# Performance work log

Hardware: AMD Instinct MI355X
Metric: run time of the kernel (lower is better)

Reference implementation:

```python
import jax, jax.numpy as jnp
import numpy as np

B, N, D = 2, 1024, 1024
H, DH = 16, 64          # nhead, head_dim (D = H*DH)
FF = 4096               # dim_feedforward = 4*D
E = 8                   # num experts
EPS = 1e-5


def layer_norm(x, s, b):
    m = jnp.mean(x, -1, keepdims=True)
    v = jnp.mean((x - m) ** 2, -1, keepdims=True)
    return (x - m) * jax.lax.rsqrt(v + EPS) * s + b


def moe_gate(x, Wg):
    # top-1 gating: expert index + gate probability per token
    probs = jax.nn.softmax(x @ Wg, axis=-1)            # [B,N,E]
    idx = jnp.argmax(probs, axis=-1)                   # [B,N]
    gw = jnp.take_along_axis(probs, idx[..., None], -1)[..., 0]  # [B,N]
    return idx, gw


def moe_linear(x, W, b, idx, gw):
    # x:[B,N,Din], W:[E,Din,Dout], b:[E,Dout]; route each token to expert idx
    y = jnp.einsum('bnd,edh->bneh', x, W) + b          # [B,N,E,Dout]
    oh = jax.nn.one_hot(idx, E, dtype=x.dtype)         # [B,N,E]
    return jnp.einsum('bneh,bne->bnh', y, oh) * gw[..., None]


def setup_inputs() -> dict:
    key = jax.random.key(0)
    ks = jax.random.split(key, 8)
    g = lambda k, shape, sc: jax.random.normal(k, shape, jnp.float32) * sc
    inv_d = 1.0 / np.sqrt(D)
    return dict(
        src=g(ks[0], (B, N, D), 1.0),
        key_padding_mask=jnp.zeros((B, N), dtype=bool),
        Wg_attn=g(ks[1], (D, E), inv_d),
        Wqkv=g(ks[2], (E, D, 3 * D), inv_d), bqkv=jnp.zeros((E, 3 * D), jnp.float32),
        Wo=g(ks[3], (E, D, D), inv_d), bo=jnp.zeros((E, D), jnp.float32),
        Wg_ffn=g(ks[4], (D, E), inv_d),
        W1=g(ks[5], (E, D, FF), inv_d), b1=jnp.zeros((E, FF), jnp.float32),
        W2=g(ks[6], (E, FF, D), 1.0 / np.sqrt(FF)), b2=jnp.zeros((E, D), jnp.float32),
        ln1_s=jnp.ones((D,), jnp.float32), ln1_b=jnp.zeros((D,), jnp.float32),
        ln2_s=jnp.ones((D,), jnp.float32), ln2_b=jnp.zeros((D,), jnp.float32),
    )


def reference(src, key_padding_mask, Wg_attn, Wqkv, bqkv, Wo, bo,
              Wg_ffn, W1, b1, W2, b2, ln1_s, ln1_b, ln2_s, ln2_b):
    # attention mask: key_padding_mask.unsqueeze(1).unsqueeze(1) * -10000
    mask = jnp.where(key_padding_mask[:, None, None, :], -10000.0, 0.0).astype(src.dtype)

    # --- MoE self-attention (gate decided once, reused for qkv and dense) ---
    idx, gw = moe_gate(src, Wg_attn)
    qkv = moe_linear(src, Wqkv, bqkv, idx, gw)                 # [B,N,3D]
    q, k, v = jnp.split(qkv, 3, axis=-1)
    heads = lambda t: t.reshape(B, N, H, DH).transpose(0, 2, 1, 3)  # [B,H,N,DH]
    q, k, v = heads(q), heads(k), heads(v)
    scores = jnp.einsum('bhqd,bhkd->bhqk', q, k) / np.sqrt(DH) + mask
    probs = jax.nn.softmax(scores, axis=-1)
    ctx = jnp.einsum('bhqk,bhkd->bhqd', probs, v)
    ctx = ctx.transpose(0, 2, 1, 3).reshape(B, N, D)
    attn_out = moe_linear(ctx, Wo, bo, idx, gw)

    # post-norm residual
    x = layer_norm(src + attn_out, ln1_s, ln1_b)

    # --- MoE FFN (its own gate, shared across both linears) ---
    fidx, fgw = moe_gate(x, Wg_ffn)
    h = jax.nn.gelu(moe_linear(x, W1, b1, fidx, fgw))
    ffn = moe_linear(h, W2, b2, fidx, fgw)

    return layer_norm(x + ffn, ln2_s, ln2_b)
```

## Files before the change

### kernel.cpp

```cpp
#include <hip/hip_runtime.h>


#define B_   2
#define N_   1024
#define D_   1024
#define H_   16
#define DH_  64
#define FF_  4096
#define E_   8
#define NTOK 2048

typedef __attribute__((ext_vector_type(8))) short short8;
typedef __attribute__((ext_vector_type(8))) unsigned short ushort8;
typedef __attribute__((ext_vector_type(4))) unsigned short ushort4v;
typedef __attribute__((ext_vector_type(4))) float f32x4;

__device__ inline unsigned short f2bf(float f) {
  unsigned u = __float_as_uint(f);
  u += 0x7FFFu + ((u >> 16) & 1u);
  return (unsigned short)(u >> 16);
}

__device__ inline float gelu_tanh(float x) {
  float x3 = x * x * x;
  float t = tanhf(0.7978845608028654f * (x + 0.044715f * x3));
  return 0.5f * x * (1.0f + t);
}

__global__ __launch_bounds__(256) void gate_kernel(
    const float* __restrict__ X, const float* __restrict__ Wg,
    int* __restrict__ idx, float* __restrict__ gwv, int* __restrict__ cnt) {
  int t = blockIdx.x * 4 + (threadIdx.x >> 6);
  int lane = threadIdx.x & 63;
  const float* x = X + (size_t)t * D_;
  float acc[E_];
#pragma unroll
  for (int j = 0; j < E_; j++) acc[j] = 0.f;
#pragma unroll
  for (int i = 0; i < 16; i++) {
    int d = i * 64 + lane;
    float xv = x[d];
    const float4* w = (const float4*)(Wg + (size_t)d * E_);
    float4 w0 = w[0], w1 = w[1];
    acc[0] += xv * w0.x; acc[1] += xv * w0.y; acc[2] += xv * w0.z; acc[3] += xv * w0.w;
    acc[4] += xv * w1.x; acc[5] += xv * w1.y; acc[6] += xv * w1.z; acc[7] += xv * w1.w;
  }
#pragma unroll
  for (int o = 1; o < 64; o <<= 1) {
#pragma unroll
    for (int j = 0; j < E_; j++) acc[j] += __shfl_xor(acc[j], o, 64);
  }
  float m = acc[0]; int bi = 0;
#pragma unroll
  for (int j = 1; j < E_; j++) { if (acc[j] > m) { m = acc[j]; bi = j; } }
  float den = 0.f;
#pragma unroll
  for (int j = 0; j < E_; j++) den += expf(acc[j] - m);
  float gw = expf(acc[bi] - m) / den;
  if (lane == 0) { idx[t] = bi; gwv[t] = gw; atomicAdd(&cnt[bi], 1); }
}

__global__ __launch_bounds__(256) void route_kernel(
    const int* __restrict__ idx, const int* __restrict__ cnt,
    int* __restrict__ off, int* __restrict__ perm, int ntok) {
  __shared__ int loff[E_ + 1];
  __shared__ int lfill[E_];
  if (threadIdx.x == 0) {
    int s = 0;
    for (int e = 0; e < E_; e++) { loff[e] = s; s += cnt[e]; }
    loff[E_] = s;
  }
  if (threadIdx.x < E_) lfill[threadIdx.x] = 0;
  __syncthreads();
  for (int t = (int)threadIdx.x; t < ntok; t += 256) {
    int e = idx[t];
    int p = atomicAdd(&lfill[e], 1);
    perm[loff[e] + p] = t;
  }
  if (threadIdx.x < E_ + 1) off[threadIdx.x] = loff[threadIdx.x];
}

__global__ __launch_bounds__(256) void cast_bf16_kernel(
    const float* __restrict__ in, unsigned short* __restrict__ out) {
  size_t i = ((size_t)blockIdx.x * 256 + threadIdx.x) * 8;
  float4 v0 = *(const float4*)(in + i);
  float4 v1 = *(const float4*)(in + i + 4);
  ushort8 o;
  o[0] = f2bf(v0.x); o[1] = f2bf(v0.y); o[2] = f2bf(v0.z); o[3] = f2bf(v0.w);
  o[4] = f2bf(v1.x); o[5] = f2bf(v1.y); o[6] = f2bf(v1.z); o[7] = f2bf(v1.w);
  *(ushort8*)(out + i) = o;
}

template <int KS>
__global__ __launch_bounds__(512, 4) void gemm_kernel(
    const unsigned short* __restrict__ A, int ldA,
    const float* __restrict__ W,
    const int* __restrict__ perm, const int* __restrict__ off,
    float* __restrict__ part, int K, int N) {
  __shared__ __align__(16) unsigned short As[2][256][32];
  __shared__ __align__(16) unsigned short Bs[128][40];
  __shared__ int toks[256];

  int e = blockIdx.y;
  int base = off[e];
  int cnt = off[e + 1] - base;
  int mt = blockIdx.z / KS;
  int kc = blockIdx.z % KS;
  int m0 = mt * 256;
  if (m0 >= cnt) return;
  int rows_valid = min(256, cnt - m0);
  int tid = threadIdx.x;
  if (tid < 256) {
    int r = (tid < rows_valid) ? tid : (rows_valid - 1);
    toks[tid] = perm[base + m0 + r];
  }
  int nb = blockIdx.x * 128;
  int lane = tid & 63, wave = tid >> 6;
  int wm = (wave & 3) * 64, wn = (wave >> 2) * 64;
  int lr = lane & 15, lg = lane >> 4;
  f32x4 acc[4][4];
#pragma unroll
  for (int m = 0; m < 4; m++)
#pragma unroll
    for (int n = 0; n < 4; n++) acc[m][n] = (f32x4){0.f, 0.f, 0.f, 0.f};

  int a_rowl = lane >> 2, a_j = lane & 3;
  int ar0 = wave * 32 + a_rowl;
  int kb2 = (tid & 15) * 2, n0 = (tid >> 4) * 4;

  int KL = K / KS, kbeg = kc * KL, kend = kbeg + KL;
  __syncthreads();

  float4 r0, r1;
  {
#pragma unroll
    for (int i = 0; i < 2; i++) {
      int row = ar0 + i * 16;
      int s = (row >> 1) & 3;
      const unsigned short* g = A + (size_t)toks[row] * ldA + kbeg + ((a_j ^ s) << 3);
      __builtin_amdgcn_global_load_lds(
          (const __attribute__((address_space(1))) unsigned int*)g,
          (__attribute__((address_space(3))) unsigned int*)&As[0][wave * 32 + i * 16][0],
          16, 0, 0);
    }
    const float* w0 = W + ((size_t)e * K + kbeg + kb2) * N + nb + n0;
    r0 = *(const float4*)w0;
    r1 = *(const float4*)(w0 + N);
  }

  int buf = 0;
  for (int k0 = kbeg; k0 < kend; k0 += 32) {
    {
      float lo[4] = {r0.x, r0.y, r0.z, r0.w};
      float hi[4] = {r1.x, r1.y, r1.z, r1.w};
#pragma unroll
      for (int j = 0; j < 4; j++) {
        int n = n0 + j;
        int sc = (((kb2 >> 3) ^ ((n >> 2) & 3)) << 3) | (kb2 & 7);
        unsigned v = (unsigned)f2bf(lo[j]) | ((unsigned)f2bf(hi[j]) << 16);
        *(unsigned*)&Bs[n][sc] = v;
      }
    }
    __syncthreads();
    if (k0 + 32 < kend) {
      int kn = k0 + 32;
#pragma unroll
      for (int i = 0; i < 2; i++) {
        int row = ar0 + i * 16;
        int s = (row >> 1) & 3;
        const unsigned short* g = A + (size_t)toks[row] * ldA + kn + ((a_j ^ s) << 3);
        __builtin_amdgcn_global_load_lds(
            (const __attribute__((address_space(1))) unsigned int*)g,
            (__attribute__((address_space(3))) unsigned int*)&As[buf ^ 1][wave * 32 + i * 16][0],
            16, 0, 0);
      }
      const float* w0 = W + ((size_t)e * K + kn + kb2) * N + nb + n0;
      r0 = *(const float4*)w0;
      r1 = *(const float4*)(w0 + N);
    }
    short8 av[4];
#pragma unroll
    for (int m = 0; m < 4; m++) {
      int r = wm + m * 16 + lr;
      av[m] = *(const short8*)&As[buf][r][(lg ^ ((r >> 1) & 3)) << 3];
    }
#pragma unroll
    for (int n = 0; n < 4; n++) {
      int nn = wn + n * 16 + lr;
      short8 bv = *(const short8*)&Bs[nn][(lg ^ ((nn >> 2) & 3)) << 3];
#pragma unroll
      for (int m = 0; m < 4; m++)
        acc[m][n] = __builtin_amdgcn_mfma_f32_16x16x32_bf16(av[m], bv, acc[m][n], 0, 0, 0);
    }
    __syncthreads();
    buf ^= 1;
  }

  float* pr = part + (size_t)kc * ((size_t)NTOK * N);
#pragma unroll
  for (int n = 0; n < 4; n++) {
    int col = nb + wn + n * 16 + lr;
#pragma unroll
    for (int m = 0; m < 4; m++) {
#pragma unroll
      for (int reg = 0; reg < 4; reg++) {
        int r = wm + m * 16 + lg * 4 + reg;
        if (r < rows_valid)
          pr[(size_t)toks[r] * N + col] = acc[m][n][reg];
      }
    }
  }
}

template <int KS, bool GELU, bool OBF16>
__global__ __launch_bounds__(256) void reduce_kernel(
    const float* __restrict__ part, const float* __restrict__ bias,
    const float* __restrict__ gwv, const int* __restrict__ idx,
    void* __restrict__ out, int N) {
  int t = blockIdx.y;
  int n = (blockIdx.x * 256 + threadIdx.x) * 4;
  int e = idx[t];
  float gw = gwv[t];
  const float* p = part + (size_t)t * N + n;
  float4 a = *(const float4*)p;
#pragma unroll
  for (int k = 1; k < KS; k++) {
    float4 q = *(const float4*)(p + (size_t)k * NTOK * N);
    a.x += q.x; a.y += q.y; a.z += q.z; a.w += q.w;
  }
  float4 bv = *(const float4*)(bias + (size_t)e * N + n);
  a.x = (a.x + bv.x) * gw; a.y = (a.y + bv.y) * gw;
  a.z = (a.z + bv.z) * gw; a.w = (a.w + bv.w) * gw;
  if constexpr (GELU) {
    a.x = gelu_tanh(a.x); a.y = gelu_tanh(a.y);
    a.z = gelu_tanh(a.z); a.w = gelu_tanh(a.w);
  }
  if constexpr (OBF16) {
    ushort4v o;
    o[0] = f2bf(a.x); o[1] = f2bf(a.y); o[2] = f2bf(a.z); o[3] = f2bf(a.w);
    *(ushort4v*)((unsigned short*)out + (size_t)t * N + n) = o;
  } else {
    *(float4*)((float*)out + (size_t)t * N + n) = a;
  }
}

__global__ __launch_bounds__(256) void vtrans_kernel(
    const unsigned short* __restrict__ qkv, unsigned short* __restrict__ vT) {
  __shared__ __align__(16) unsigned short T[64][72];
  int bh = blockIdx.x;
  int b = bh >> 4, h = bh & 15;
  int tile = blockIdx.y;
  int tid = threadIdx.x;
  {
    int tk = tid >> 2, dof = (tid & 3) * 16;
    const unsigned short* p =
        qkv + ((size_t)(b * N_ + tile * 64 + tk)) * 3072 + 2048 + h * 64 + dof;
    *(ushort8*)&T[tk][dof] = *(const ushort8*)p;
    *(ushort8*)&T[tk][dof + 8] = *(const ushort8*)(p + 8);
  }
  __syncthreads();
  {
    int dh = tid >> 2, tof = (tid & 3) * 16;
    ushort8 o0, o1;
#pragma unroll
    for (int i = 0; i < 8; i++) o0[i] = T[tof + i][dh];
#pragma unroll
    for (int i = 0; i < 8; i++) o1[i] = T[tof + 8 + i][dh];
    unsigned short* q = vT + ((size_t)bh * 64 + dh) * N_ + tile * 64 + tof;
    *(ushort8*)q = o0;
    *(ushort8*)(q + 8) = o1;
  }
}

__global__ __launch_bounds__(256) void attn_kernel(
    const unsigned short* __restrict__ qkv, const unsigned short* __restrict__ vT,
    const unsigned char* __restrict__ kpm, unsigned short* __restrict__ ctx) {
  __shared__ __align__(16) unsigned short Qs[64][72];
  __shared__ __align__(16) unsigned short Ks[64][72];
  __shared__ __align__(16) unsigned short Vs[64][72];
  __shared__ __align__(16) unsigned short Ps[4][16][72];
  __shared__ float maskf[64];
  int qt = blockIdx.x, bh = blockIdx.y;
  int b = bh >> 4, h = bh & 15;
  int tid = threadIdx.x, lane = tid & 63, wave = tid >> 6;
  int lr = lane & 15, lg = lane >> 4;
  {
    int r = tid >> 2, dof = (tid & 3) * 16;
    const unsigned short* p = qkv + ((size_t)(b * N_ + qt * 64 + r)) * 3072 + h * 64 + dof;
    *(ushort8*)&Qs[r][dof] = *(const ushort8*)p;
    *(ushort8*)&Qs[r][dof + 8] = *(const ushort8*)(p + 8);
  }
  __syncthreads();
  short8 aq[2];
  aq[0] = *(const short8*)&Qs[wave * 16 + lr][lg * 8];
  aq[1] = *(const short8*)&Qs[wave * 16 + lr][32 + lg * 8];
  f32x4 O[4];
  float mrun[4], lrun[4];
#pragma unroll
  for (int r = 0; r < 4; r++) { mrun[r] = -1e30f; lrun[r] = 0.f; O[r] = (f32x4){0.f, 0.f, 0.f, 0.f}; }

  for (int kt = 0; kt < 16; kt++) {
    __syncthreads();
    {
      int r = tid >> 2, dof = (tid & 3) * 16;
      const unsigned short* p =
          qkv + ((size_t)(b * N_ + kt * 64 + r)) * 3072 + 1024 + h * 64 + dof;
      *(ushort8*)&Ks[r][dof] = *(const ushort8*)p;
      *(ushort8*)&Ks[r][dof + 8] = *(const ushort8*)(p + 8);
      const unsigned short* pv = vT + ((size_t)bh * 64 + r) * N_ + kt * 64 + dof;
      *(ushort8*)&Vs[r][dof] = *(const ushort8*)pv;
      *(ushort8*)&Vs[r][dof + 8] = *(const ushort8*)(pv + 8);
      if (tid < 64) maskf[tid] = kpm[b * N_ + kt * 64 + tid] ? -10000.f : 0.f;
    }
    __syncthreads();
    f32x4 S[4];
#pragma unroll
    for (int n = 0; n < 4; n++) {
      f32x4 s = (f32x4){0.f, 0.f, 0.f, 0.f};
#pragma unroll
      for (int ks = 0; ks < 2; ks++) {
        short8 bk = *(const short8*)&Ks[n * 16 + lr][ks * 32 + lg * 8];
        s = __builtin_amdgcn_mfma_f32_16x16x32_bf16(aq[ks], bk, s, 0, 0, 0);
      }
      float mv = maskf[n * 16 + lr];
#pragma unroll
      for (int r = 0; r < 4; r++) s[r] = s[r] * 0.125f + mv;
      S[n] = s;
    }
    float cur[4];
#pragma unroll
    for (int r = 0; r < 4; r++)
      cur[r] = fmaxf(fmaxf(S[0][r], S[1][r]), fmaxf(S[2][r], S[3][r]));
#pragma unroll
    for (int o = 1; o < 16; o <<= 1) {
#pragma unroll
      for (int r = 0; r < 4; r++) cur[r] = fmaxf(cur[r], __shfl_xor(cur[r], o, 64));
    }
    float alpha[4], rsum[4];
#pragma unroll
    for (int r = 0; r < 4; r++) {
      float mn = fmaxf(mrun[r], cur[r]);
      alpha[r] = expf(mrun[r] - mn);
      mrun[r] = mn;
      rsum[r] = 0.f;
    }
#pragma unroll
    for (int n = 0; n < 4; n++) {
#pragma unroll
      for (int r = 0; r < 4; r++) {
        S[n][r] = expf(S[n][r] - mrun[r]);
        rsum[r] += S[n][r];
      }
    }
#pragma unroll
    for (int o = 1; o < 16; o <<= 1) {
#pragma unroll
      for (int r = 0; r < 4; r++) rsum[r] += __shfl_xor(rsum[r], o, 64);
    }
#pragma unroll
    for (int r = 0; r < 4; r++) lrun[r] = lrun[r] * alpha[r] + rsum[r];
#pragma unroll
    for (int d = 0; d < 4; d++)
#pragma unroll
      for (int r = 0; r < 4; r++) O[d][r] *= alpha[r];
#pragma unroll
    for (int n = 0; n < 4; n++)
#pragma unroll
      for (int r = 0; r < 4; r++) Ps[wave][lg * 4 + r][n * 16 + lr] = f2bf(S[n][r]);
    short8 pf[2];
    pf[0] = *(const short8*)&Ps[wave][lr][lg * 8];
    pf[1] = *(const short8*)&Ps[wave][lr][32 + lg * 8];
#pragma unroll
    for (int d = 0; d < 4; d++) {
#pragma unroll
      for (int ks = 0; ks < 2; ks++) {
        short8 bv = *(const short8*)&Vs[d * 16 + lr][ks * 32 + lg * 8];
        O[d] = __builtin_amdgcn_mfma_f32_16x16x32_bf16(pf[ks], bv, O[d], 0, 0, 0);
      }
    }
  }
#pragma unroll
  for (int r = 0; r < 4; r++) lrun[r] = 1.f / lrun[r];
#pragma unroll
  for (int d = 0; d < 4; d++) {
#pragma unroll
    for (int r = 0; r < 4; r++) {
      int q = qt * 64 + wave * 16 + lg * 4 + r;
      int dh = d * 16 + lr;
      ctx[((size_t)(b * N_ + q)) * D_ + h * DH_ + dh] = f2bf(O[d][r] * lrun[r]);
    }
  }
}

template <int KS, bool WBF>
__global__ __launch_bounds__(256) void ln_reduce_kernel(
    const float* __restrict__ res, const float* __restrict__ part,
    const float* __restrict__ bias, const float* __restrict__ gwv,
    const int* __restrict__ idx,
    const float* __restrict__ S, const float* __restrict__ Bi,
    float* __restrict__ O, unsigned short* __restrict__ Obf) {
  int t = blockIdx.x, tid = threadIdx.x;
  int e = idx[t];
  float gw = gwv[t];
  const float* p = part + (size_t)t * D_ + tid * 4;
  float4 a = *(const float4*)p;
#pragma unroll
  for (int k = 1; k < KS; k++) {
    float4 q = *(const float4*)(p + (size_t)k * NTOK * D_);
    a.x += q.x; a.y += q.y; a.z += q.z; a.w += q.w;
  }
  float4 bv4 = *(const float4*)(bias + (size_t)e * D_ + tid * 4);
  float4 vr = ((const float4*)(res + (size_t)t * D_))[tid];
  float4 v;
  v.x = vr.x + (a.x + bv4.x) * gw;
  v.y = vr.y + (a.y + bv4.y) * gw;
  v.z = vr.z + (a.z + bv4.z) * gw;
  v.w = vr.w + (a.w + bv4.w) * gw;
  float s = v.x + v.y + v.z + v.w;
  float sq = v.x * v.x + v.y * v.y + v.z * v.z + v.w * v.w;
#pragma unroll
  for (int o = 1; o < 64; o <<= 1) {
    s += __shfl_xor(s, o, 64);
    sq += __shfl_xor(sq, o, 64);
  }
  __shared__ float ss[4], ssq[4];
  int wave = tid >> 6, lane = tid & 63;
  if (lane == 0) { ss[wave] = s; ssq[wave] = sq; }
  __syncthreads();
  float ts = ss[0] + ss[1] + ss[2] + ss[3];
  float tsq = ssq[0] + ssq[1] + ssq[2] + ssq[3];
  float mean = ts * (1.f / D_);
  float var = tsq * (1.f / D_) - mean * mean;
  float rs = rsqrtf(var + 1e-5f);
  float4 sv = ((const float4*)S)[tid];
  float4 bi = ((const float4*)Bi)[tid];
  float4 o;
  o.x = (v.x - mean) * rs * sv.x + bi.x;
  o.y = (v.y - mean) * rs * sv.y + bi.y;
  o.z = (v.z - mean) * rs * sv.z + bi.z;
  o.w = (v.w - mean) * rs * sv.w + bi.w;
  ((float4*)(O + (size_t)t * D_))[tid] = o;
  if constexpr (WBF) {
    ushort4v ob;
    ob[0] = f2bf(o.x); ob[1] = f2bf(o.y); ob[2] = f2bf(o.z); ob[3] = f2bf(o.w);
    *(ushort4v*)(Obf + (size_t)t * D_ + tid * 4) = ob;
  }
}

extern "C" void kernel_launch(void* const* d_in, const int* in_sizes, int n_in,
                              void* d_out, int out_size, void* d_ws, size_t ws_size,
                              hipStream_t stream) {
  (void)in_sizes; (void)n_in; (void)out_size; (void)ws_size;
  const float* src     = (const float*)d_in[0];
  const unsigned char* kpm = (const unsigned char*)d_in[1];
  const float* Wg_attn = (const float*)d_in[2];
  const float* Wqkv    = (const float*)d_in[3];
  const float* bqkv    = (const float*)d_in[4];
  const float* Wo      = (const float*)d_in[5];
  const float* bo      = (const float*)d_in[6];
  const float* Wg_ffn  = (const float*)d_in[7];
  const float* W1      = (const float*)d_in[8];
  const float* b1      = (const float*)d_in[9];
  const float* W2      = (const float*)d_in[10];
  const float* b2      = (const float*)d_in[11];
  const float* ln1_s   = (const float*)d_in[12];
  const float* ln1_b   = (const float*)d_in[13];
  const float* ln2_s   = (const float*)d_in[14];
  const float* ln2_b   = (const float*)d_in[15];
  float* out = (float*)d_out;

  char* ws = (char*)d_ws;
  size_t o = 0;
  auto alloc = [&](size_t bytes) -> void* {
    void* p = ws + o;
    o += (bytes + 255) & ~(size_t)255;
    return p;
  };
  int* meta = (int*)alloc(256);
  int* cnt1 = meta;
  int* off1 = meta + 8;
  int* cnt2 = meta + 17;
  int* off2 = meta + 25;
  int* idx1 = (int*)alloc(NTOK * 4);
  float* gw1 = (float*)alloc(NTOK * 4);
  int* perm1 = (int*)alloc(NTOK * 4);
  int* idx2 = (int*)alloc(NTOK * 4);
  float* gw2 = (float*)alloc(NTOK * 4);
  int* perm2 = (int*)alloc(NTOK * 4);
  unsigned short* qkvb = (unsigned short*)alloc((size_t)NTOK * 3072 * 2);
  unsigned short* vT = (unsigned short*)alloc((size_t)32 * 64 * N_ * 2);
  unsigned short* hbuf = qkvb;
  unsigned short* ctx = (unsigned short*)alloc((size_t)NTOK * D_ * 2);
  unsigned short* src_bf = ctx;
  unsigned short* x_bf = ctx;
  float* x = (float*)alloc((size_t)NTOK * D_ * 4);
  float* part = (float*)alloc((size_t)2 * NTOK * FF_ * 4);

  hipMemsetAsync(meta, 0, 256, stream);

  cast_bf16_kernel<<<1024, 256, 0, stream>>>(src, src_bf);
  gate_kernel<<<512, 256, 0, stream>>>(src, Wg_attn, idx1, gw1, cnt1);
  route_kernel<<<1, 256, 0, stream>>>(idx1, cnt1, off1, perm1, NTOK);
  gemm_kernel<2><<<dim3(3072 / 128, 8, 16), 512, 0, stream>>>(
      src_bf, 1024, Wqkv, perm1, off1, part, 1024, 3072);
  reduce_kernel<2, false, true><<<dim3(3, NTOK), 256, 0, stream>>>(
      part, bqkv, gw1, idx1, qkvb, 3072);
  vtrans_kernel<<<dim3(32, 16), 256, 0, stream>>>(qkvb, vT);
  attn_kernel<<<dim3(16, 32), 256, 0, stream>>>(qkvb, vT, kpm, ctx);
  gemm_kernel<4><<<dim3(1024 / 128, 8, 32), 512, 0, stream>>>(
      ctx, 1024, Wo, perm1, off1, part, 1024, 1024);
  ln_reduce_kernel<4, true><<<NTOK, 256, 0, stream>>>(
      src, part, bo, gw1, idx1, ln1_s, ln1_b, x, x_bf);

  gate_kernel<<<512, 256, 0, stream>>>(x, Wg_ffn, idx2, gw2, cnt2);
  route_kernel<<<1, 256, 0, stream>>>(idx2, cnt2, off2, perm2, NTOK);
  gemm_kernel<2><<<dim3(4096 / 128, 8, 16), 512, 0, stream>>>(
      x_bf, 1024, W1, perm2, off2, part, 1024, 4096);
  reduce_kernel<2, true, true><<<dim3(4, NTOK), 256, 0, stream>>>(
      part, b1, gw2, idx2, hbuf, 4096);
  gemm_kernel<4><<<dim3(1024 / 128, 8, 32), 512, 0, stream>>>(
      hbuf, 4096, W2, perm2, off2, part, 4096, 1024);
  ln_reduce_kernel<4, false><<<NTOK, 256, 0, stream>>>(
      x, part, b2, gw2, idx2, ln2_s, ln2_b, out, (unsigned short*)nullptr);
}
```

Measured before the change: 672.4 us.

## Restructure MoE GEMM to 128-row tiles with register-staged double-buffered loads

```diff
diff --git a/kernel.cpp b/kernel.cpp
--- a/kernel.cpp
+++ b/kernel.cpp
@@ -14,6 +14,7 @@
 typedef __attribute__((ext_vector_type(8))) unsigned short ushort8;
 typedef __attribute__((ext_vector_type(4))) unsigned short ushort4v;
 typedef __attribute__((ext_vector_type(4))) float f32x4;
+typedef __attribute__((ext_vector_type(2))) unsigned int uint32x2;
 
 __device__ inline unsigned short f2bf(float f) {
   unsigned u = __float_as_uint(f);
@@ -92,109 +93,124 @@
 }
 
 template <int KS>
-__global__ __launch_bounds__(512, 4) void gemm_kernel(
+__global__ __launch_bounds__(256, 3) void gemm_kernel(
     const unsigned short* __restrict__ A, int ldA,
     const float* __restrict__ W,
     const int* __restrict__ perm, const int* __restrict__ off,
     float* __restrict__ part, int K, int N) {
-  __shared__ __align__(16) unsigned short As[2][256][32];
+  __shared__ __align__(16) unsigned short As[128][32];
   __shared__ __align__(16) unsigned short Bs[128][40];
-  __shared__ int toks[256];
+  __shared__ int toks[128];
 
   int e = blockIdx.y;
   int base = off[e];
   int cnt = off[e + 1] - base;
   int mt = blockIdx.z / KS;
   int kc = blockIdx.z % KS;
-  int m0 = mt * 256;
+  int m0 = mt * 128;
   if (m0 >= cnt) return;
-  int rows_valid = min(256, cnt - m0);
+  int rows_valid = min(128, cnt - m0);
   int tid = threadIdx.x;
-  if (tid < 256) {
+  if (tid < 128) {
     int r = (tid < rows_valid) ? tid : (rows_valid - 1);
     toks[tid] = perm[base + m0 + r];
   }
   int nb = blockIdx.x * 128;
   int lane = tid & 63, wave = tid >> 6;
-  int wm = (wave & 3) * 64, wn = (wave >> 2) * 64;
+  int wm = (wave & 1) * 64, wn = (wave >> 1) * 64;
   int lr = lane & 15, lg = lane >> 4;
+  int aswz = (lg ^ ((lr >> 1) & 3)) << 3;
+  int bswz = (lg ^ ((lr >> 2) & 3)) << 3;
+
   f32x4 acc[4][4];
 #pragma unroll
   for (int m = 0; m < 4; m++)
 #pragma unroll
     for (int n = 0; n < 4; n++) acc[m][n] = (f32x4){0.f, 0.f, 0.f, 0.f};
 
-  int a_rowl = lane >> 2, a_j = lane & 3;
-  int ar0 = wave * 32 + a_rowl;
-  int kb2 = (tid & 15) * 2, n0 = (tid >> 4) * 4;
-
-  int KL = K / KS, kbeg = kc * KL, kend = kbeg + KL;
+  int arow = tid >> 1;
+  int aj0 = (tid & 1) * 2;
+  int as_ = (arow >> 1) & 3;
+  int k4 = (tid & 7) * 4, n0 = (tid >> 3) * 4;
+
+  int KL = K / KS, kbeg = kc * KL;
+  int nt = KL / 32;
   __syncthreads();
 
-  float4 r0, r1;
-  {
-#pragma unroll
-    for (int i = 0; i < 2; i++) {
-      int row = ar0 + i * 16;
-      int s = (row >> 1) & 3;
-      const unsigned short* g = A + (size_t)toks[row] * ldA + kbeg + ((a_j ^ s) << 3);
-      __builtin_amdgcn_global_load_lds(
-          (const __attribute__((address_space(1))) unsigned int*)g,
-          (__attribute__((address_space(3))) unsigned int*)&As[0][wave * 32 + i * 16][0],
-          16, 0, 0);
-    }
-    const float* w0 = W + ((size_t)e * K + kbeg + kb2) * N + nb + n0;
-    r0 = *(const float4*)w0;
-    r1 = *(const float4*)(w0 + N);
-  }
-
-  int buf = 0;
-  for (int k0 = kbeg; k0 < kend; k0 += 32) {
-    {
-      float lo[4] = {r0.x, r0.y, r0.z, r0.w};
-      float hi[4] = {r1.x, r1.y, r1.z, r1.w};
-#pragma unroll
-      for (int j = 0; j < 4; j++) {
-        int n = n0 + j;
-        int sc = (((kb2 >> 3) ^ ((n >> 2) & 3)) << 3) | (kb2 & 7);
-        unsigned v = (unsigned)f2bf(lo[j]) | ((unsigned)f2bf(hi[j]) << 16);
-        *(unsigned*)&Bs[n][sc] = v;
-      }
-    }
-    __syncthreads();
-    if (k0 + 32 < kend) {
-      int kn = k0 + 32;
-#pragma unroll
-      for (int i = 0; i < 2; i++) {
-        int row = ar0 + i * 16;
-        int s = (row >> 1) & 3;
-        const unsigned short* g = A + (size_t)toks[row] * ldA + kn + ((a_j ^ s) << 3);
-        __builtin_amdgcn_global_load_lds(
-            (const __attribute__((address_space(1))) unsigned int*)g,
-            (__attribute__((address_space(3))) unsigned int*)&As[buf ^ 1][wave * 32 + i * 16][0],
-            16, 0, 0);
-      }
-      const float* w0 = W + ((size_t)e * K + kn + kb2) * N + nb + n0;
-      r0 = *(const float4*)w0;
-      r1 = *(const float4*)(w0 + N);
-    }
-    short8 av[4];
-#pragma unroll
-    for (int m = 0; m < 4; m++) {
-      int r = wm + m * 16 + lr;
-      av[m] = *(const short8*)&As[buf][r][(lg ^ ((r >> 1) & 3)) << 3];
-    }
-#pragma unroll
-    for (int n = 0; n < 4; n++) {
-      int nn = wn + n * 16 + lr;
-      short8 bv = *(const short8*)&Bs[nn][(lg ^ ((nn >> 2) & 3)) << 3];
-#pragma unroll
-      for (int m = 0; m < 4; m++)
-        acc[m][n] = __builtin_amdgcn_mfma_f32_16x16x32_bf16(av[m], bv, acc[m][n], 0, 0, 0);
-    }
-    __syncthreads();
-    buf ^= 1;
-  }
+  const unsigned short* abase = A + (size_t)toks[arow] * ldA + aj0 * 8;
+  const float* wbase = W + ((size_t)e * K + k4) * N + nb + n0;
+
+  ushort8 aR0, aR1;
+  f32x4 bA0, bA1, bA2, bA3, bB0, bB1, bB2, bB3;
+
+#define LOAD_A(KK) {                                                      \
+    const unsigned short* ap = abase + (KK);                              \
+    aR0 = *(const ushort8*)ap;                                            \
+    aR1 = *(const ushort8*)(ap + 8); }
+
+#define LOAD_B(KK, R0, R1, R2, R3) {                                      \
+    const float* wp = wbase + (size_t)(KK) * N;                           \
+    R0 = *(const f32x4*)wp;                                               \
+    R1 = *(const f32x4*)(wp + N);                                         \
+    R2 = *(const f32x4*)(wp + 2 * N);                                     \
+    R3 = *(const f32x4*)(wp + 3 * N); }
+
+#define PUBLISH(R0, R1, R2, R3) {                                         \
+    *(ushort8*)&As[arow][(aj0 ^ as_) << 3] = aR0;                         \
+    *(ushort8*)&As[arow][((aj0 + 1) ^ as_) << 3] = aR1;                   \
+    _Pragma("unroll")                                                     \
+    for (int j = 0; j < 4; j++) {                                         \
+      int n = n0 + j;                                                     \
+      int bb = (((k4 >> 3) ^ ((n >> 2) & 3)) << 3) | (k4 & 7);            \
+      unsigned lo = (unsigned)f2bf(R0[j]) | ((unsigned)f2bf(R1[j]) << 16);\
+      unsigned hi = (unsigned)f2bf(R2[j]) | ((unsigned)f2bf(R3[j]) << 16);\
+      *(uint32x2*)&Bs[n][bb] = (uint32x2){lo, hi};                        \
+    } }
+
+#define COMPUTE() {                                                       \
+    short8 av[4], bv[4];                                                  \
+    _Pragma("unroll")                                                     \
+    for (int m = 0; m < 4; m++)                                           \
+      av[m] = *(const short8*)&As[wm + m * 16 + lr][aswz];                \
+    _Pragma("unroll")                                                     \
+    for (int n = 0; n < 4; n++)                                           \
+      bv[n] = *(const short8*)&Bs[wn + n * 16 + lr][bswz];                \
+    __builtin_amdgcn_s_setprio(1);                                        \
+    _Pragma("unroll")                                                     \
+    for (int n = 0; n < 4; n++)                                           \
+      _Pragma("unroll")                                                   \
+      for (int m = 0; m < 4; m++)                                         \
+        acc[m][n] = __builtin_amdgcn_mfma_f32_16x16x32_bf16(              \
+            av[m], bv[n], acc[m][n], 0, 0, 0);                            \
+    __builtin_amdgcn_s_setprio(0); }
+
+  LOAD_A(kbeg);
+  LOAD_B(kbeg, bA0, bA1, bA2, bA3);
+  if (nt > 1) LOAD_B(kbeg + 32, bB0, bB1, bB2, bB3);
+
+  for (int t = 0; t < nt; t += 2) {
+    int k0 = kbeg + t * 32;
+    PUBLISH(bA0, bA1, bA2, bA3);
+    if (t + 1 < nt) LOAD_A(k0 + 32);
+    if (t + 2 < nt) LOAD_B(k0 + 64, bA0, bA1, bA2, bA3);
+    asm volatile("s_waitcnt lgkmcnt(0)" ::: "memory");
+    __builtin_amdgcn_s_barrier();
+    COMPUTE();
+    __builtin_amdgcn_s_barrier();
+    if (t + 1 < nt) {
+      PUBLISH(bB0, bB1, bB2, bB3);
+      if (t + 2 < nt) LOAD_A(k0 + 64);
+      if (t + 3 < nt) LOAD_B(k0 + 96, bB0, bB1, bB2, bB3);
+      asm volatile("s_waitcnt lgkmcnt(0)" ::: "memory");
+      __builtin_amdgcn_s_barrier();
+      COMPUTE();
+      __builtin_amdgcn_s_barrier();
+    }
+  }
+#undef LOAD_A
+#undef LOAD_B
+#undef PUBLISH
+#undef COMPUTE
 
   float* pr = part + (size_t)kc * ((size_t)NTOK * N);
 #pragma unroll
@@ -501,24 +517,24 @@
   cast_bf16_kernel<<<1024, 256, 0, stream>>>(src, src_bf);
   gate_kernel<<<512, 256, 0, stream>>>(src, Wg_attn, idx1, gw1, cnt1);
   route_kernel<<<1, 256, 0, stream>>>(idx1, cnt1, off1, perm1, NTOK);
-  gemm_kernel<2><<<dim3(3072 / 128, 8, 16), 512, 0, stream>>>(
+  gemm_kernel<2><<<dim3(3072 / 128, 8, 32), 256, 0, stream>>>(
       src_bf, 1024, Wqkv, perm1, off1, part, 1024, 3072);
   reduce_kernel<2, false, true><<<dim3(3, NTOK), 256, 0, stream>>>(
       part, bqkv, gw1, idx1, qkvb, 3072);
   vtrans_kernel<<<dim3(32, 16), 256, 0, stream>>>(qkvb, vT);
   attn_kernel<<<dim3(16, 32), 256, 0, stream>>>(qkvb, vT, kpm, ctx);
-  gemm_kernel<4><<<dim3(1024 / 128, 8, 32), 512, 0, stream>>>(
+  gemm_kernel<4><<<dim3(1024 / 128, 8, 64), 256, 0, stream>>>(
       ctx, 1024, Wo, perm1, off1, part, 1024, 1024);
   ln_reduce_kernel<4, true><<<NTOK, 256, 0, stream>>>(
       src, part, bo, gw1, idx1, ln1_s, ln1_b, x, x_bf);
 
   gate_kernel<<<512, 256, 0, stream>>>(x, Wg_ffn, idx2, gw2, cnt2);
   route_kernel<<<1, 256, 0, stream>>>(idx2, cnt2, off2, perm2, NTOK);
-  gemm_kernel<2><<<dim3(4096 / 128, 8, 16), 512, 0, stream>>>(
+  gemm_kernel<2><<<dim3(4096 / 128, 8, 32), 256, 0, stream>>>(
       x_bf, 1024, W1, perm2, off2, part, 1024, 4096);
   reduce_kernel<2, true, true><<<dim3(4, NTOK), 256, 0, stream>>>(
       part, b1, gw2, idx2, hbuf, 4096);
-  gemm_kernel<4><<<dim3(1024 / 128, 8, 32), 512, 0, stream>>>(
+  gemm_kernel<4><<<dim3(8, 8, 64), 256, 0, stream>>>(
       hbuf, 4096, W2, perm2, off2, part, 4096, 1024);
   ln_reduce_kernel<4, false><<<NTOK, 256, 0, stream>>>(
       x, part, b2, gw2, idx2, ln2_s, ln2_b, out, (unsigned short*)nullptr);
```

New measurement: 698.9 us. +3.9%, slower.
